# Optimization experiments

Measured on AMD Instinct MI355X. Metric: run time of the kernel, lower is better.

## Reference

```python
import jax, jax.numpy as jnp
import numpy as np

B, N, C = 8, 2048, 64  # batch, num nodes, channels
DENSITY = 0.01


def setup_inputs() -> dict:
    key = jax.random.key(0)
    k = jax.random.split(key, 8)
    x = jax.random.normal(k[0], (B, N, C), dtype=jnp.float32)

    # --- replicate sym_norm_Adj(Adj_matrix) + row softmax from __init__ ---
    W = (jax.random.uniform(k[1], (N, N)) < DENSITY).astype(jnp.float32)
    W = W + 0.5 * jnp.eye(N, dtype=jnp.float32)          # W + 0.5*I
    deg = jnp.sum((W != 0.0).astype(jnp.float32), axis=1)  # row nonzero counts
    A = jnp.sqrt(deg)[:, None] * W * jnp.sqrt(deg)[None, :]  # sqrt(D) W sqrt(D)
    A = jax.nn.softmax(A, axis=1)

    s = 1.0 / np.sqrt(C)
    Wq = jax.random.normal(k[2], (C, C), dtype=jnp.float32) * s   # stored as (in,out)
    Wk = jax.random.normal(k[3], (C, C), dtype=jnp.float32) * s
    Wv = jax.random.normal(k[4], (C, N), dtype=jnp.float32) * s   # c_in -> num_node
    theta_w = jax.random.normal(k[5], (C, C), dtype=jnp.float32) * s
    theta_b = jnp.zeros((C,), dtype=jnp.float32)
    alpha = jnp.array([0.95], dtype=jnp.float32)
    beta = jnp.array([0.95], dtype=jnp.float32)
    return {"x": x, "A": A, "Wq": Wq, "Wk": Wk, "Wv": Wv,
            "theta_w": theta_w, "theta_b": theta_b, "alpha": alpha, "beta": beta}


def reference(x, A, Wq, Wk, Wv, theta_w, theta_b, alpha, beta):
    # Spatial_Attention_layer
    Q = x @ Wq                                   # (B,N,C)
    K = x @ Wk                                   # (B,N,C)
    V = x @ Wv                                   # (B,N,N)
    score = jnp.einsum('bnc,bmc->bnm', Q, K)     # (B,N,N)
    score = jax.nn.softmax(score, axis=1)        # softmax over dim=1 (as in torch code)
    spat = jnp.einsum('bnm,bmk->bnk', score, V)  # (B,N,N) spatial attention

    # einsum('nn,bnc->bnc', A, x) == diag(A) broadcast-multiply
    static_out = jnp.diagonal(A)[None, :, None] * x  # (B,N,C)

    # dy_adj = A @ spat; einsum('bnn,bnc->bnc', dy_adj, x) uses only diag(dy_adj)
    dy_diag = jnp.einsum('nj,bjn->bn', A, spat)      # (B,N), avoids (B,N,N) intermediate
    dy_out = (dy_diag[:, :, None] * x) @ theta_w + theta_b  # Theta1 linear

    out = jax.nn.relu(alpha[0] * static_out + beta[0] * dy_out)
    return out
```

## Files before the change

kernel.cpp:

```cpp
#include <hip/hip_runtime.h>

constexpr int Bb = 8;
constexpr int Nn = 2048;
constexpr int Cc = 64;
constexpr int CAPS = 192;

typedef __attribute__((ext_vector_type(4))) float f32x4;
typedef __attribute__((ext_vector_type(16))) float f32x16;
typedef __attribute__((ext_vector_type(8))) short bf16x8;
typedef __attribute__((ext_vector_type(4))) unsigned u32x4;

__device__ inline unsigned short f2bf(float f){
  unsigned u = __builtin_bit_cast(unsigned, f);
  unsigned r = (u + 0x7FFFu + ((u>>16)&1u)) >> 16;
  return (unsigned short)r;
}
__device__ inline float bf2f(unsigned short h){
  unsigned u = ((unsigned)h)<<16; return __builtin_bit_cast(float,u);
}
__device__ inline unsigned pk2(float a, float b){
  return (unsigned)f2bf(a) | ((unsigned)f2bf(b)<<16);
}

typedef __attribute__((address_space(1))) unsigned GU32;
typedef __attribute__((address_space(3))) unsigned LU32;
__device__ inline void load_lds16(const void* g, void* l){
  __builtin_amdgcn_global_load_lds((const GU32*)g, (LU32*)l, 16, 0, 0);
}

#define PIPE_FENCE_N(N) do{ \
    asm volatile("s_waitcnt vmcnt(" #N ")" ::: "memory"); \
    __builtin_amdgcn_sched_barrier(0); \
    __builtin_amdgcn_s_barrier(); \
    __builtin_amdgcn_sched_barrier(0); }while(0)

__device__ inline size_t qk_chunk(int b, int s, int q, int l){
  return ((((size_t)b*64 + s)*4 + q)*64 + l)*8;
}
__device__ inline size_t xz_chunk(int b, int mq, int cb, int l){
  return ((((size_t)b*128 + mq)*2 + cb)*64 + l)*8;
}

#define MFMA32(a,b,c) __builtin_amdgcn_mfma_f32_32x32x16_bf16(a,b,c,0,0,0)

__global__ __launch_bounds__(256) void mega_k(
    const float* __restrict__ x, const float* __restrict__ A,
    const float* __restrict__ Wq, const float* __restrict__ Wk,
    const float* __restrict__ Tw, const float* __restrict__ Wv,
    unsigned short* __restrict__ Qhi, unsigned short* __restrict__ Qlo,
    unsigned short* __restrict__ Khi, unsigned short* __restrict__ Klo,
    float* __restrict__ xt, float* __restrict__ Xp,
    float* __restrict__ r_, float* __restrict__ diagA, int* __restrict__ cnt,
    int* __restrict__ idx, float* __restrict__ val,
    float* __restrict__ WvT, unsigned short* __restrict__ xf){
  __shared__ __attribute__((aligned(16))) char smem[65792];
  int blk = blockIdx.x; int t = threadIdx.x;

  if(blk < 256){
    float* wql = (float*)smem;
    float* wkl = wql + 4096;
    float* twl = wkl + 4096;
    float (*xr)[64] = (float(*)[64])(twl + 4096);
    float* xsl = (float*)(xr + 64);
    #pragma unroll
    for(int i=0;i<4;i++){
      *(f32x4*)&wql[i*1024+t*4] = *(const f32x4*)&Wq[i*1024+t*4];
      *(f32x4*)&wkl[i*1024+t*4] = *(const f32x4*)&Wk[i*1024+t*4];
      *(f32x4*)&twl[i*1024+t*4] = *(const f32x4*)&Tw[i*1024+t*4];
    }
    if(t<64) xsl[t]=0.f;
    long long row0 = (long long)blk*64;
    int r = t>>4, q = t&15, c0 = q*4;
    #pragma unroll
    for(int i=0;i<4;i++){
      int row = i*16 + r;
      *(f32x4*)&xr[row][c0] = *(const f32x4*)&x[(row0+row)*Cc + c0];
    }
    __syncthreads();
    f32x4 aq[4], ak[4], at4[4];
    #pragma unroll
    for(int g=0;g<4;g++){ aq[g]=(f32x4){0,0,0,0}; ak[g]=(f32x4){0,0,0,0}; at4[g]=(f32x4){0,0,0,0}; }
    for(int kk=0;kk<64;kk++){
      f32x4 wq4 = *(const f32x4*)&wql[kk*64+c0];
      f32x4 wk4 = *(const f32x4*)&wkl[kk*64+c0];
      f32x4 wt4 = *(const f32x4*)&twl[kk*64+c0];
      #pragma unroll
      for(int g=0;g<4;g++){
        float xv = xr[g*16+r][kk];
        aq[g] += xv*wq4; ak[g] += xv*wk4; at4[g] += xv*wt4;
      }
    }
    float xsp[4] = {0.f,0.f,0.f,0.f};
    int q2 = c0>>4, hb = (c0>>3)&1, cs = c0&7;
    #pragma unroll
    for(int g=0;g<4;g++){
      #pragma unroll
      for(int d=0;d<4;d++) xsp[d] += xr[g*16+r][c0+d];
      long long rg = row0 + g*16 + r;
      unsigned long long hq=0,lq=0,hk=0,lk=0;
      #pragma unroll
      for(int d=0;d<4;d++){
        float v = aq[g][d];
        unsigned short h = f2bf(v); unsigned short lo2 = f2bf(v - bf2f(h));
        hq |= (unsigned long long)h << (16*d); lq |= (unsigned long long)lo2 << (16*d);
        v = ak[g][d];
        h = f2bf(v); lo2 = f2bf(v - bf2f(h));
        hk |= (unsigned long long)h << (16*d); lk |= (unsigned long long)lo2 << (16*d);
      }
      int b2 = (int)(rg>>11); int s2 = ((int)rg>>5)&63;
      int l2 = ((int)rg&31) + 32*hb;
      size_t off = qk_chunk(b2, s2, q2, l2) + cs;
      *(unsigned long long*)&Qhi[off] = hq;
      *(unsigned long long*)&Qlo[off] = lq;
      *(unsigned long long*)&Khi[off] = hk;
      *(unsigned long long*)&Klo[off] = lk;
      *(f32x4*)&xt[rg*Cc + c0] = at4[g];
    }
    __syncthreads();
    #pragma unroll
    for(int d=0;d<4;d++) atomicAdd(&xsl[c0+d], xsp[d]);
    __syncthreads();
    if(t<64) Xp[blk*64+t] = xsl[t];
    {
      int b2 = blk>>5; int m0 = (blk&31)*64;
      #pragma unroll
      for(int i=0;i<2;i++){
        int k2 = i*256 + t; int mg2 = k2>>6; int c = k2&63;
        int mloc = mg2*8;
        unsigned u0 = pk2(xr[mloc+0][c], xr[mloc+1][c]);
        unsigned u1 = pk2(xr[mloc+2][c], xr[mloc+3][c]);
        unsigned u2 = pk2(xr[mloc+4][c], xr[mloc+5][c]);
        unsigned u3 = pk2(xr[mloc+6][c], xr[mloc+7][c]);
        u32x4 uu = {u0,u1,u2,u3};
        int mq = (m0 + mloc)>>4; int cb = c>>5; int l2 = (c&31) + 32*(mg2&1);
        *(u32x4*)(xf + xz_chunk(b2, mq, cb, l2)) = uu;
      }
    }
  } else if(blk < 768){
    int n = (blk-256)*4 + (t>>6); int l = t&63;
    const float* row = A + (size_t)n*Nn;
    float mn = 1e30f;
    for(int j=l;j<Nn;j+=64) mn = fminf(mn, row[j]);
    #pragma unroll
    for(int off=32;off>=1;off>>=1) mn = fminf(mn, __shfl_xor(mn,off));
    float thr = mn*1.3f;
    int bse=0;
    for(int j0=0;j0<Nn;j0+=64){
      float v = row[j0+l];
      bool f = v>thr;
      unsigned long long m = __ballot(f);
      int pos = __popcll(m & ((1ull<<l)-1ull));
      if(f && bse+pos<CAPS){ idx[n*CAPS+bse+pos]=j0+l; val[n*CAPS+bse+pos]=v-mn; }
      bse += __popcll(m);
    }
    if(l==0){ r_[n]=mn; diagA[n]=row[n]; cnt[n] = bse<CAPS? bse : CAPS; }
  } else {
    float (*tile)[65] = (float(*)[65])smem;
    int n0 = (blk-768)*64;
    for(int i=0;i<16;i++){
      int cc = i*4 + (t>>6); int nn2 = t&63;
      tile[cc][nn2] = Wv[(size_t)cc*Nn + n0 + nn2];
    }
    __syncthreads();
    for(int i=0;i<16;i++){
      int nn2 = i*4 + (t>>6); int cc = t&63;
      WvT[(size_t)(n0+nn2)*Cc + cc] = tile[cc][nn2];
    }
  }
}

__global__ __launch_bounds__(256,2) void zpass_k(
    const unsigned short* __restrict__ Qhi, const unsigned short* __restrict__ Qlo,
    const unsigned short* __restrict__ Khi, const unsigned short* __restrict__ Klo,
    float* __restrict__ Zp){
  __shared__ uint4 stg[3][512];
  int id = blockIdx.x;
  int b = id&7; int mg = (id>>3)&15; int jq = id>>7;
  int t = threadIdx.x, w = t>>6, l = t&63;
  int mt = mg*4 + w;
  bf16x8 Kh[4], Kl4[4];
  #pragma unroll
  for(int q=0;q<4;q++){
    Kh[q]  = *(const bf16x8*)(Khi + qk_chunk(b, mt, q, l));
    Kl4[q] = *(const bf16x8*)(Klo + qk_chunk(b, mt, q, l));
  }
#define ZISSUE(S, BI) { \
    char* wb = (char*)&stg[BI][0] + ((t>>6)<<10); \
    load_lds16(Qhi + qk_chunk(b,(S),0,0) + t*8, wb); \
    load_lds16(Qlo + qk_chunk(b,(S),0,0) + t*8, wb + 4096); }
  ZISSUE(jq*8,   0);
  ZISSUE(jq*8+1, 1);
  float zacc = 0.f;
  #pragma unroll
  for(int it=0; it<8; it++){
    const int bi = it%3;
    if(it==7) PIPE_FENCE_N(0); else PIPE_FENCE_N(2);
    f32x16 sa, sb;
    #pragma unroll
    for(int r=0;r<16;r++){ sa[r]=0.f; sb[r]=0.f; }
    #pragma unroll
    for(int q=0;q<4;q++){
      bf16x8 Qh4 = *(const bf16x8*)&stg[bi][q*64 + l];
      bf16x8 Ql4 = *(const bf16x8*)&stg[bi][256 + q*64 + l];
      sa = MFMA32(Qh4, Kh[q],  sa);
      sb = MFMA32(Ql4, Kh[q],  sb);
      sb = MFMA32(Qh4, Kl4[q], sb);
    }
    float p = 0.f;
    #pragma unroll
    for(int r=0;r<16;r++) p += __expf(sa[r]+sb[r]);
    zacc += p;
    if(it+2<8) ZISSUE(jq*8+it+2, (it+2)%3);
  }
#undef ZISSUE
  zacc += __shfl_down(zacc, 32);
  if(l<32) Zp[((size_t)(jq*8 + b))*Nn + mt*32 + l] = zacc;
}

__global__ __launch_bounds__(256,2) void fused_k(
    const unsigned short* __restrict__ Qhi, const unsigned short* __restrict__ Qlo,
    const unsigned short* __restrict__ Khi, const unsigned short* __restrict__ Klo,
    const unsigned short* __restrict__ xf, const float* __restrict__ Zp,
    float* __restrict__ Pp){
  __shared__ uint4 stg[3][768];
  __shared__ float lniz[512];
  int id = blockIdx.x;
  int b = id&7; int jb = (id>>3)&15; int mo = id>>7;
  int t = threadIdx.x, w = t>>6, l = t&63, lr = l&31, hh = l>>5;
  int js = jb*4 + w;
  #pragma unroll
  for(int i=0;i<2;i++){
    int m = mo*512 + i*256 + t;
    float z = 0.f;
    #pragma unroll
    for(int p=0;p<8;p++) z += Zp[((size_t)(p*8 + b))*Nn + m];
    lniz[i*256+t] = -__logf(z);
  }
  bf16x8 Qh4[4], Ql4[4];
  #pragma unroll
  for(int q=0;q<4;q++){
    Qh4[q] = *(const bf16x8*)(Qhi + qk_chunk(b, js, q, l));
    Ql4[q] = *(const bf16x8*)(Qlo + qk_chunk(b, js, q, l));
  }
  __syncthreads();
#define FISSUE(S, BI) { \
    char* wb = (char*)&stg[BI][0] + ((t>>6)<<10); \
    load_lds16(Khi + qk_chunk(b,(S),0,0) + t*8, wb); \
    load_lds16(Klo + qk_chunk(b,(S),0,0) + t*8, wb + 4096); \
    load_lds16(xf + xz_chunk(b,2*(S),0,0) + t*8, wb + 8192); }
  FISSUE(mo*16,   0);
  FISSUE(mo*16+1, 1);
  f32x16 pa0, pa1;
  #pragma unroll
  for(int r=0;r<16;r++){ pa0[r]=0.f; pa1[r]=0.f; }
  #pragma unroll
  for(int it=0; it<16; it++){
    const int bi = it%3;
    if(it==15) PIPE_FENCE_N(0); else PIPE_FENCE_N(3);
    f32x16 sa, sb;
    #pragma unroll
    for(int r=0;r<16;r++){ sa[r]=0.f; sb[r]=0.f; }
    #pragma unroll
    for(int q=0;q<4;q++){
      bf16x8 Kh4 = *(const bf16x8*)&stg[bi][q*64 + l];
      bf16x8 Kl4 = *(const bf16x8*)&stg[bi][256 + q*64 + l];
      sa = MFMA32(Kh4, Qh4[q], sa);
      sb = MFMA32(Kl4, Qh4[q], sb);
      sb = MFMA32(Kh4, Ql4[q], sb);
    }
    bf16x8 b00 = *(const bf16x8*)&stg[bi][512 + l];
    bf16x8 b10 = *(const bf16x8*)&stg[bi][512 + 64 + l];
    bf16x8 b01 = *(const bf16x8*)&stg[bi][512 + 128 + l];
    bf16x8 b11 = *(const bf16x8*)&stg[bi][512 + 192 + l];
    float e[16];
    #pragma unroll
    for(int r=0;r<16;r++){
      int mrow = (r&3) + 8*(r>>2) + 4*hh;
      e[r] = __expf(sa[r] + sb[r] + lniz[it*32 + mrow]);
    }
    unsigned wd0,wd1,wd2,wd3,wd4,wd5,wd6,wd7;
    {
      unsigned x0 = pk2(e[0],  e[1]);
      unsigned x1 = pk2(e[2],  e[3]);
      unsigned y0 = pk2(e[4],  e[5]);
      unsigned y1 = pk2(e[6],  e[7]);
      asm("v_permlane32_swap_b32 %0, %1" : "+v"(x0), "+v"(y0));
      asm("v_permlane32_swap_b32 %0, %1" : "+v"(x1), "+v"(y1));
      wd0=x0; wd1=x1; wd2=y0; wd3=y1;
      unsigned x2 = pk2(e[8],  e[9]);
      unsigned x3 = pk2(e[10], e[11]);
      unsigned y2 = pk2(e[12], e[13]);
      unsigned y3 = pk2(e[14], e[15]);
      asm("v_permlane32_swap_b32 %0, %1" : "+v"(x2), "+v"(y2));
      asm("v_permlane32_swap_b32 %0, %1" : "+v"(x3), "+v"(y3));
      wd4=x2; wd5=x3; wd6=y2; wd7=y3;
    }
    u32x4 u1 = {wd0,wd1,wd2,wd3};
    u32x4 u2 = {wd4,wd5,wd6,wd7};
    bf16x8 f1 = __builtin_bit_cast(bf16x8, u1);
    bf16x8 f2 = __builtin_bit_cast(bf16x8, u2);
    pa0 = MFMA32(f1, b00, pa0);
    pa0 = MFMA32(f2, b01, pa0);
    pa1 = MFMA32(f1, b10, pa1);
    pa1 = MFMA32(f2, b11, pa1);
    if(it+2<16) FISSUE(mo*16+it+2, (it+2)%3);
  }
#undef FISSUE
  float* Pb = Pp + ((size_t)(mo*8 + b)*Nn + js*32)*Cc;
  #pragma unroll
  for(int r=0;r<16;r++){
    int jr = (r&3) + 8*(r>>2) + 4*hh;
    Pb[(size_t)jr*Cc + lr]      = pa0[r];
    Pb[(size_t)jr*Cc + 32 + lr] = pa1[r];
  }
}

__global__ __launch_bounds__(256) void psum_k(const float* __restrict__ Pp,
                                              float* __restrict__ P){
  size_t i = ((size_t)blockIdx.x*256 + threadIdx.x)*4;
  const size_t st = (size_t)Bb*Nn*Cc;
  f32x4 a = *(const f32x4*)(Pp + i);
  f32x4 b = *(const f32x4*)(Pp + st + i);
  f32x4 c = *(const f32x4*)(Pp + 2*st + i);
  f32x4 d = *(const f32x4*)(Pp + 3*st + i);
  *(f32x4*)(P + i) = (a+b)+(c+d);
}

__global__ __launch_bounds__(256) void final_k(const float* __restrict__ x,
    const float* __restrict__ xt, const float* __restrict__ P,
    const float* __restrict__ WvT, const float* __restrict__ Xp,
    const float* __restrict__ r_, const float* __restrict__ diagA,
    const int* __restrict__ cnt, const int* __restrict__ idx,
    const float* __restrict__ val, const float* __restrict__ tb,
    const float* __restrict__ alp, const float* __restrict__ bet,
    float* __restrict__ out){
  int t=threadIdx.x; int l=t&63;
  int bn = blockIdx.x*4 + (t>>6);
  int b = bn>>11, n = bn&2047;
  float wv = WvT[n*Cc+l];
  float xs = 0.f;
  const float* xpb = Xp + (size_t)b*32*Cc;
  #pragma unroll 8
  for(int p=0;p<32;p++) xs += xpb[p*Cc + l];
  float tacc = r_[n]*xs;
  int cn = cnt[n];
  const float* Pb = P + (size_t)b*Nn*Cc;
  const int* ix = idx + n*CAPS;
  const float* vl = val + n*CAPS;
  for(int k=0;k<cn;k++)
    tacc += vl[k] * Pb[(size_t)ix[k]*Cc + l];
  float d = wv*tacc;
  #pragma unroll
  for(int off=32;off>=1;off>>=1) d += __shfl_xor(d,off);
  size_t g = (size_t)bn*Cc + l;
  float o = alp[0]*diagA[n]*x[g] + bet[0]*(d*xt[g] + tb[l]);
  out[g] = fmaxf(o,0.f);
}

extern "C" void kernel_launch(void* const* d_in, const int* in_sizes, int n_in,
                              void* d_out, int out_size, void* d_ws, size_t ws_size,
                              hipStream_t stream){
  const float* x  = (const float*)d_in[0];
  const float* A  = (const float*)d_in[1];
  const float* Wq = (const float*)d_in[2];
  const float* Wk = (const float*)d_in[3];
  const float* Wv = (const float*)d_in[4];
  const float* Tw = (const float*)d_in[5];
  const float* tb = (const float*)d_in[6];
  const float* alp= (const float*)d_in[7];
  const float* bet= (const float*)d_in[8];
  float* out = (float*)d_out;

  char* base = (char*)d_ws; size_t off=0;
  auto al=[&](size_t sz)->void*{ void* q = base+off; off=(off+sz+255)&~(size_t)255; return q; };
  unsigned short* Qhi=(unsigned short*)al((size_t)Bb*Nn*Cc*2);
  unsigned short* Qlo=(unsigned short*)al((size_t)Bb*Nn*Cc*2);
  unsigned short* Khi=(unsigned short*)al((size_t)Bb*Nn*Cc*2);
  unsigned short* Klo=(unsigned short*)al((size_t)Bb*Nn*Cc*2);
  float* xt  =(float*)al((size_t)Bb*Nn*Cc*4);
  float* Pp  =(float*)al((size_t)4*Bb*Nn*Cc*4);
  float* P   =(float*)al((size_t)Bb*Nn*Cc*4);
  float* Zp  =(float*)al((size_t)8*Bb*Nn*4);
  float* Xp  =(float*)al((size_t)256*Cc*4);
  float* WvT =(float*)al((size_t)Nn*Cc*4);
  float* r_  =(float*)al((size_t)Nn*4);
  float* dgA =(float*)al((size_t)Nn*4);
  int*   cnt =(int*)al((size_t)Nn*4);
  int*   idx =(int*)al((size_t)Nn*CAPS*4);
  float* val =(float*)al((size_t)Nn*CAPS*4);
  unsigned short* xf=(unsigned short*)al((size_t)Bb*Cc*Nn*2);
  (void)ws_size; (void)n_in; (void)in_sizes; (void)out_size;

  mega_k<<<800, 256, 0, stream>>>(x, A, Wq, Wk, Tw, Wv,
      Qhi, Qlo, Khi, Klo, xt, Xp, r_, dgA, cnt, idx, val, WvT, xf);
  zpass_k<<<1024, 256, 0, stream>>>(Qhi,Qlo,Khi,Klo,Zp);
  fused_k<<<512, 256, 0, stream>>>(Qhi,Qlo,Khi,Klo,xf,Zp,Pp);
  psum_k<<<(int)((size_t)Bb*Nn*Cc/4/256), 256, 0, stream>>>(Pp,P);
  final_k<<<Bb*Nn/4, 256, 0, stream>>>(x,xt,P,WvT,Xp,r_,dgA,cnt,idx,val,tb,alp,bet,out);
}
```

Measured before the change: 107.5 us.

## Merge four post-setup kernels into one cooperative kernel with grid syncs

Replaces the zpass, fused, psum and final kernel launches with a single cooperative kernel of 512 blocks. The phases are separated by grid.sync(), and each block handles two zpass units and several final rows. The aim is to remove the launch overhead and inter-kernel gaps between the four stages. In exchange, grid-wide barriers are added, the zpass and final phases run on fewer blocks, and the code falls back to the old launches if the cooperative launch fails.

```diff
diff --git a/kernel.cpp b/kernel.cpp
--- a/kernel.cpp
+++ b/kernel.cpp
@@ -1,4 +1,7 @@
 #include <hip/hip_runtime.h>
+#include <hip/hip_cooperative_groups.h>
+
+namespace cg = cooperative_groups;
 
 constexpr int Bb = 8;
 constexpr int Nn = 2048;
@@ -166,6 +169,198 @@
       int nn2 = i*4 + (t>>6); int cc = t&63;
       WvT[(size_t)(n0+nn2)*Cc + cc] = tile[cc][nn2];
     }
+  }
+}
+
+__global__ __launch_bounds__(256,2) void coop_k(
+    const unsigned short* __restrict__ Qhi, const unsigned short* __restrict__ Qlo,
+    const unsigned short* __restrict__ Khi, const unsigned short* __restrict__ Klo,
+    const unsigned short* __restrict__ xf, float* __restrict__ Zp,
+    float* __restrict__ Pp, float* __restrict__ P,
+    const float* __restrict__ x, const float* __restrict__ xt,
+    const float* __restrict__ WvT, const float* __restrict__ Xp,
+    const float* __restrict__ r_, const float* __restrict__ diagA,
+    const int* __restrict__ cnt, const int* __restrict__ idx,
+    const float* __restrict__ val, const float* __restrict__ tb,
+    const float* __restrict__ alp, const float* __restrict__ bet,
+    float* __restrict__ out){
+  cg::grid_group grid = cg::this_grid();
+  __shared__ uint4 stg[3][768];
+  __shared__ float lniz[512];
+  int id = blockIdx.x;
+  int t = threadIdx.x, w = t>>6, l = t&63, lr = l&31, hh = l>>5;
+
+  for(int u=0; u<2; u++){
+    int unit = id*2 + u;
+    int b = unit&7; int mg = (unit>>3)&15; int jq = unit>>7;
+    int mt = mg*4 + w;
+    bf16x8 Kh[4], Kl4[4];
+    #pragma unroll
+    for(int q=0;q<4;q++){
+      Kh[q]  = *(const bf16x8*)(Khi + qk_chunk(b, mt, q, l));
+      Kl4[q] = *(const bf16x8*)(Klo + qk_chunk(b, mt, q, l));
+    }
+    __syncthreads();
+#define CZISSUE(S, BI) { \
+    char* wb = (char*)&stg[BI][0] + ((t>>6)<<10); \
+    load_lds16(Qhi + qk_chunk(b,(S),0,0) + t*8, wb); \
+    load_lds16(Qlo + qk_chunk(b,(S),0,0) + t*8, wb + 4096); }
+    CZISSUE(jq*8,   0);
+    CZISSUE(jq*8+1, 1);
+    float zacc = 0.f;
+    #pragma unroll
+    for(int it=0; it<8; it++){
+      const int bi = it%3;
+      if(it==7) PIPE_FENCE_N(0); else PIPE_FENCE_N(2);
+      f32x16 sa, sb;
+      #pragma unroll
+      for(int r=0;r<16;r++){ sa[r]=0.f; sb[r]=0.f; }
+      #pragma unroll
+      for(int q=0;q<4;q++){
+        bf16x8 Qh4 = *(const bf16x8*)&stg[bi][q*64 + l];
+        bf16x8 Ql4 = *(const bf16x8*)&stg[bi][256 + q*64 + l];
+        sa = MFMA32(Qh4, Kh[q],  sa);
+        sb = MFMA32(Ql4, Kh[q],  sb);
+        sb = MFMA32(Qh4, Kl4[q], sb);
+      }
+      float p = 0.f;
+      #pragma unroll
+      for(int r=0;r<16;r++) p += __expf(sa[r]+sb[r]);
+      zacc += p;
+      if(it+2<8) CZISSUE(jq*8+it+2, (it+2)%3);
+    }
+#undef CZISSUE
+    zacc += __shfl_down(zacc, 32);
+    if(l<32) Zp[((size_t)(jq*8 + b))*Nn + mt*32 + l] = zacc;
+  }
+  grid.sync();
+
+  {
+    int b = id&7; int jb = (id>>3)&15; int mo = id>>7;
+    int js = jb*4 + w;
+    #pragma unroll
+    for(int i=0;i<2;i++){
+      int m = mo*512 + i*256 + t;
+      float z = 0.f;
+      #pragma unroll
+      for(int p=0;p<8;p++) z += Zp[((size_t)(p*8 + b))*Nn + m];
+      lniz[i*256+t] = -__logf(z);
+    }
+    bf16x8 Qh4[4], Ql4[4];
+    #pragma unroll
+    for(int q=0;q<4;q++){
+      Qh4[q] = *(const bf16x8*)(Qhi + qk_chunk(b, js, q, l));
+      Ql4[q] = *(const bf16x8*)(Qlo + qk_chunk(b, js, q, l));
+    }
+    __syncthreads();
+#define CFISSUE(S, BI) { \
+    char* wb = (char*)&stg[BI][0] + ((t>>6)<<10); \
+    load_lds16(Khi + qk_chunk(b,(S),0,0) + t*8, wb); \
+    load_lds16(Klo + qk_chunk(b,(S),0,0) + t*8, wb + 4096); \
+    load_lds16(xf + xz_chunk(b,2*(S),0,0) + t*8, wb + 8192); }
+    CFISSUE(mo*16,   0);
+    CFISSUE(mo*16+1, 1);
+    f32x16 pa0, pa1;
+    #pragma unroll
+    for(int r=0;r<16;r++){ pa0[r]=0.f; pa1[r]=0.f; }
+    #pragma unroll
+    for(int it=0; it<16; it++){
+      const int bi = it%3;
+      if(it==15) PIPE_FENCE_N(0); else PIPE_FENCE_N(3);
+      f32x16 sa, sb;
+      #pragma unroll
+      for(int r=0;r<16;r++){ sa[r]=0.f; sb[r]=0.f; }
+      #pragma unroll
+      for(int q=0;q<4;q++){
+        bf16x8 Kh4 = *(const bf16x8*)&stg[bi][q*64 + l];
+        bf16x8 Kl4 = *(const bf16x8*)&stg[bi][256 + q*64 + l];
+        sa = MFMA32(Kh4, Qh4[q], sa);
+        sb = MFMA32(Kl4, Qh4[q], sb);
+        sb = MFMA32(Kh4, Ql4[q], sb);
+      }
+      bf16x8 b00 = *(const bf16x8*)&stg[bi][512 + l];
+      bf16x8 b10 = *(const bf16x8*)&stg[bi][512 + 64 + l];
+      bf16x8 b01 = *(const bf16x8*)&stg[bi][512 + 128 + l];
+      bf16x8 b11 = *(const bf16x8*)&stg[bi][512 + 192 + l];
+      float e[16];
+      #pragma unroll
+      for(int r=0;r<16;r++){
+        int mrow = (r&3) + 8*(r>>2) + 4*hh;
+        e[r] = __expf(sa[r] + sb[r] + lniz[it*32 + mrow]);
+      }
+      unsigned wd0,wd1,wd2,wd3,wd4,wd5,wd6,wd7;
+      {
+        unsigned x0 = pk2(e[0],  e[1]);
+        unsigned x1 = pk2(e[2],  e[3]);
+        unsigned y0 = pk2(e[4],  e[5]);
+        unsigned y1 = pk2(e[6],  e[7]);
+        asm("v_permlane32_swap_b32 %0, %1" : "+v"(x0), "+v"(y0));
+        asm("v_permlane32_swap_b32 %0, %1" : "+v"(x1), "+v"(y1));
+        wd0=x0; wd1=x1; wd2=y0; wd3=y1;
+        unsigned x2 = pk2(e[8],  e[9]);
+        unsigned x3 = pk2(e[10], e[11]);
+        unsigned y2 = pk2(e[12], e[13]);
+        unsigned y3 = pk2(e[14], e[15]);
+        asm("v_permlane32_swap_b32 %0, %1" : "+v"(x2), "+v"(y2));
+        asm("v_permlane32_swap_b32 %0, %1" : "+v"(x3), "+v"(y3));
+        wd4=x2; wd5=x3; wd6=y2; wd7=y3;
+      }
+      u32x4 u1 = {wd0,wd1,wd2,wd3};
+      u32x4 u2 = {wd4,wd5,wd6,wd7};
+      bf16x8 f1 = __builtin_bit_cast(bf16x8, u1);
+      bf16x8 f2 = __builtin_bit_cast(bf16x8, u2);
+      pa0 = MFMA32(f1, b00, pa0);
+      pa0 = MFMA32(f2, b01, pa0);
+      pa1 = MFMA32(f1, b10, pa1);
+      pa1 = MFMA32(f2, b11, pa1);
+      if(it+2<16) CFISSUE(mo*16+it+2, (it+2)%3);
+    }
+#undef CFISSUE
+    float* Pb = Pp + ((size_t)(mo*8 + b)*Nn + js*32)*Cc;
+    #pragma unroll
+    for(int r=0;r<16;r++){
+      int jr = (r&3) + 8*(r>>2) + 4*hh;
+      Pb[(size_t)jr*Cc + lr]      = pa0[r];
+      Pb[(size_t)jr*Cc + 32 + lr] = pa1[r];
+    }
+  }
+  grid.sync();
+
+  {
+    const size_t st = (size_t)Bb*Nn*Cc;
+    #pragma unroll
+    for(int g2=0; g2<2; g2++){
+      size_t i = ((size_t)id*512 + g2*256 + t)*4;
+      f32x4 a = *(const f32x4*)(Pp + i);
+      f32x4 b = *(const f32x4*)(Pp + st + i);
+      f32x4 c = *(const f32x4*)(Pp + 2*st + i);
+      f32x4 d = *(const f32x4*)(Pp + 3*st + i);
+      *(f32x4*)(P + i) = (a+b)+(c+d);
+    }
+  }
+  grid.sync();
+
+  for(int rep=0; rep<8; rep++){
+    int bn = rep*2048 + id*4 + w;
+    int b = bn>>11, n = bn&2047;
+    float wv = WvT[n*Cc+l];
+    float xs = 0.f;
+    const float* xpb = Xp + (size_t)b*32*Cc;
+    #pragma unroll 8
+    for(int p=0;p<32;p++) xs += xpb[p*Cc + l];
+    float tacc = r_[n]*xs;
+    int cn = cnt[n];
+    const float* Pb = P + (size_t)b*Nn*Cc;
+    const int* ix = idx + n*CAPS;
+    const float* vl = val + n*CAPS;
+    for(int k=0;k<cn;k++)
+      tacc += vl[k] * Pb[(size_t)ix[k]*Cc + l];
+    float d = wv*tacc;
+    #pragma unroll
+    for(int off=32;off>=1;off>>=1) d += __shfl_xor(d,off);
+    size_t g = (size_t)bn*Cc + l;
+    float o = alp[0]*diagA[n]*x[g] + bet[0]*(d*xt[g] + tb[l]);
+    out[g] = fmaxf(o,0.f);
   }
 }
 
@@ -393,8 +588,20 @@
 
   mega_k<<<800, 256, 0, stream>>>(x, A, Wq, Wk, Tw, Wv,
       Qhi, Qlo, Khi, Klo, xt, Xp, r_, dgA, cnt, idx, val, WvT, xf);
-  zpass_k<<<1024, 256, 0, stream>>>(Qhi,Qlo,Khi,Klo,Zp);
-  fused_k<<<512, 256, 0, stream>>>(Qhi,Qlo,Khi,Klo,xf,Zp,Pp);
-  psum_k<<<(int)((size_t)Bb*Nn*Cc/4/256), 256, 0, stream>>>(Pp,P);
-  final_k<<<Bb*Nn/4, 256, 0, stream>>>(x,xt,P,WvT,Xp,r_,dgA,cnt,idx,val,tb,alp,bet,out);
-}
+
+  void* args[] = {
+    (void*)&Qhi, (void*)&Qlo, (void*)&Khi, (void*)&Klo,
+    (void*)&xf, (void*)&Zp, (void*)&Pp, (void*)&P,
+    (void*)&x, (void*)&xt, (void*)&WvT, (void*)&Xp,
+    (void*)&r_, (void*)&dgA, (void*)&cnt, (void*)&idx,
+    (void*)&val, (void*)&tb, (void*)&alp, (void*)&bet, (void*)&out
+  };
+  hipError_t e = hipLaunchCooperativeKernel((const void*)coop_k, dim3(512),
+                                            dim3(256), args, 0, stream);
+  if(e != hipSuccess){
+    zpass_k<<<1024, 256, 0, stream>>>(Qhi,Qlo,Khi,Klo,Zp);
+    fused_k<<<512, 256, 0, stream>>>(Qhi,Qlo,Khi,Klo,xf,Zp,Pp);
+    psum_k<<<(int)((size_t)Bb*Nn*Cc/4/256), 256, 0, stream>>>(Pp,P);
+    final_k<<<Bb*Nn/4, 256, 0, stream>>>(x,xt,P,WvT,Xp,r_,dgA,cnt,idx,val,tb,alp,bet,out);
+  }
+}
```

New measurement: 341.0 us. +217.1%, slower.
